# Kernel tuning notes

Hardware: AMD Instinct MI355X
Metric: run time of the kernel (lower is better)

## Reference

```python
import jax, jax.numpy as jnp
import numpy as np

# Module hyperparameters (match init_kwargs)
E, H = 16, 8          # embedding_dim, n_head
DI, DO = 8, 8         # dim_in, dim_out (voices)
F = 48                # num_frames_in = num_frames_out = max_num_frames
L_IN, L_OUT = F * DI, F * DO
SZ_B = 4              # batch size (q has SZ_B * H leading dim)


def _expand(mat):
    # mat: (F, F, E, H) -> (L_IN, L_OUT, E, H), block expansion over voices
    e = jnp.tile(mat, (1, DI, 1, 1))                 # (F, DI*F, E, H)
    f = e.reshape(DI * F, F, E, H)                   # (L_IN, F, E, H)
    g = jnp.transpose(f, (1, 0, 2, 3))               # (F, L_IN, E, H)
    h = jnp.tile(g, (1, DO, 1, 1))                   # (F, DO*L_IN, E, H)
    ret = jnp.transpose(h.reshape(DO * F, DI * F, E, H), (1, 0, 2, 3))
    return ret[:L_IN, :L_OUT]


def _prepare_r_time(inp, is_future):
    # inp: (F, E, H). Skewing trick via pad + tile + reshape (faithful to torch).
    a = jnp.concatenate([inp, jnp.full((1, E, H), -111.0, inp.dtype)], axis=0)  # (F+1, E, H)
    b = jnp.tile(a[None], (F, 1, 1, 1))              # (F, F+1, E, H)
    c = b.reshape(F + 1, F, E, H)
    d = c[:F] if is_future else jnp.transpose(c[:F], (1, 0, 2, 3))  # (F, F, E, H)
    return _expand(d)


def _preprocess(r_voice, e_past, e_future):
    one = jnp.ones((F, F), r_voice.dtype)
    mask_past = jnp.broadcast_to(jnp.tril(one)[:, :, None, None], (F, F, E, H))
    mask_future = jnp.broadcast_to(jnp.triu(one, 1)[:, :, None, None], (F, F, E, H))
    r_voice_rep = jnp.tile(r_voice, (F, F, 1, 1))    # (L_IN, L_OUT, E, H)
    r_time = (_expand(mask_past) * _prepare_r_time(e_past, False)
              + _expand(mask_future) * _prepare_r_time(e_future, True))
    return r_voice_rep, r_time


def setup_inputs() -> dict:
    key = jax.random.key(0)
    k1, k2, k3, k4 = jax.random.split(key, 4)
    return {
        "q": jax.random.normal(k1, (SZ_B * H, L_IN, E), jnp.float32),
        "flipped_masks": jnp.zeros((1,), jnp.int32),  # unused by forward
        "r_voice": jax.random.normal(k2, (DI, DO, E, H), jnp.float32),
        "e_past": jax.random.normal(k3, (F, E, H), jnp.float32),
        "e_future": jax.random.normal(k4, (F, E, H), jnp.float32),
    }


def reference(q, flipped_masks, r_voice, e_past, e_future):
    rv, rt = _preprocess(r_voice, e_past, e_future)
    # torch: permute(3,0,1,2) then repeat over batch -> (b*H, L, M, E) with index b*H + h.
    # Equivalent without the batch repeat: reshape q to (b, H, L, E) and einsum over heads.
    rv = jnp.transpose(rv, (3, 0, 1, 2))             # (H, L_IN, L_OUT, E)
    rt = jnp.transpose(rt, (3, 0, 1, 2))
    qb = q.reshape(SZ_B, H, L_IN, E)
    # use_voice_attention=True: rel_attn_instrument + rel_attn_time (single fused einsum)
    rel = jnp.einsum('bhld,hlmd->bhlm', qb, rv + rt)
    return rel.reshape(SZ_B * H, L_IN, L_OUT)
```

## Files before the change

kernel.cpp:

```cpp
#include <hip/hip_runtime.h>
#include <hip/hip_bf16.h>

#define E_DIM 16
#define H_DIM 8
#define F_DIM 48
#define L_IN 384
#define L_OUT 384
#define SZ_B 4

#define NCHUNK 8
#define ROWS_PER_BLOCK 48
#define FI_PER 6
#define TSTRIDE 20

typedef float f32x4 __attribute__((ext_vector_type(4)));

__global__ __launch_bounds__(512)
void bsa_fused_kernel(const float* __restrict__ q,
                      const float* __restrict__ r_voice,
                      const float* __restrict__ e_past,
                      const float* __restrict__ e_future,
                      float* __restrict__ out) {
    const int chunk = blockIdx.x;
    const int bh    = blockIdx.y;
    const int h     = bh & (H_DIM - 1);
    const int t     = threadIdx.x;
    const int w     = t >> 6;
    const int lane  = t & 63;

    __shared__ __attribute__((aligned(16))) float tabs[160 * TSTRIDE];
    __shared__ __attribute__((aligned(16))) float qs[ROWS_PER_BLOCK * E_DIM];
    __shared__ __attribute__((aligned(16))) float scratch[8 * 64];

    for (int i = t; i < F_DIM * E_DIM; i += 512) {
        const int f = i >> 4, d = i & 15;
        tabs[f * TSTRIDE + d]           = e_past [(size_t)i * H_DIM + h];
        tabs[(F_DIM + f) * TSTRIDE + d] = e_future[(size_t)i * H_DIM + h];
    }
    for (int i = t; i < 64 * E_DIM; i += 512) {
        const int r = i >> 4, d = i & 15;
        tabs[(96 + r) * TSTRIDE + d] = r_voice[(size_t)i * H_DIM + h];
    }
    for (int i = t; i < ROWS_PER_BLOCK * E_DIM; i += 512)
        qs[i] = q[((size_t)bh * L_IN + chunk * ROWS_PER_BLOCK) * E_DIM + i];
    __syncthreads();

    float* wscratch = &scratch[w * 64];

    for (int j = 0; j < FI_PER; ++j) {
        const int lrow = w * FI_PER + j;
        const int l    = chunk * ROWS_PER_BLOCK + lrow;
        const int fi   = l >> 3;
        const int vi   = l & 7;

        int r;
        if (lane < 48) {
            r = (lane <= fi) ? (fi - lane) : (F_DIM + lane - fi);
        } else {
            int vj = (lane - 48) & 7;
            r = 96 + vi * 8 + vj;
        }
        const f32x4* qv = (const f32x4*)&qs[lrow * E_DIM];
        const f32x4* tv = (const f32x4*)&tabs[r * TSTRIDE];
        f32x4 acc = qv[0] * tv[0] + qv[1] * tv[1] + qv[2] * tv[2] + qv[3] * tv[3];
        const float s = acc.x + acc.y + acc.z + acc.w;
        if (lane < 56) wscratch[lane] = s;
        asm volatile("s_waitcnt lgkmcnt(0)" ::: "memory");
        __builtin_amdgcn_wave_barrier();

        float* orow = out + ((size_t)bh * L_IN + l) * L_OUT;
        #pragma unroll
        for (int rr = 0; rr < 2; ++rr) {
            const int jj = rr * 64 + lane;
            if (jj < 96) {
                const float tval = wscratch[jj >> 1];
                const f32x4 vv = *(const f32x4*)&wscratch[48 + 4 * (jj & 1)];
                f32x4 o;
                o.x = tval + vv.x; o.y = tval + vv.y;
                o.z = tval + vv.z; o.w = tval + vv.w;
                __builtin_nontemporal_store(o, (f32x4*)(orow + 4 * jj));
            }
        }
        __builtin_amdgcn_wave_barrier();
    }
}

extern "C" void kernel_launch(void* const* d_in, const int* in_sizes, int n_in,
                              void* d_out, int out_size, void* d_ws, size_t ws_size,
                              hipStream_t stream) {
    const float* q        = (const float*)d_in[0];
    const float* r_voice  = (const float*)d_in[2];
    const float* e_past   = (const float*)d_in[3];
    const float* e_future = (const float*)d_in[4];
    float* out = (float*)d_out;

    dim3 grid(NCHUNK, SZ_B * H_DIM);
    bsa_fused_kernel<<<grid, dim3(512), 0, stream>>>(q, r_voice, e_past, e_future, out);
}
```

Before: 10.78 us.

## Halve block size, double grid, batch dot products before stores, drop nontemporal

Moves to 256-thread blocks covering 24 rows each, doubling the grid to 512 blocks so more CUs share the work. Each wave now computes all six rows' dot products into per-row scratch first, then does one wave barrier and issues all output stores, instead of alternating compute, barrier and store per row. Nontemporal stores are replaced by normal stores. In exchange, the per-head tables are loaded into LDS twice as many times overall, and losing the nontemporal hint may change how the output write stream interacts with the cache.

```diff
diff --git a/kernel.cpp b/kernel.cpp
--- a/kernel.cpp
+++ b/kernel.cpp
@@ -8,14 +8,14 @@
 #define L_OUT 384
 #define SZ_B 4
 
-#define NCHUNK 8
-#define ROWS_PER_BLOCK 48
-#define FI_PER 6
+#define NCHUNK 16
+#define ROWS_PER_BLOCK 24
+#define ROWS_PER_WAVE 6
 #define TSTRIDE 20
 
 typedef float f32x4 __attribute__((ext_vector_type(4)));
 
-__global__ __launch_bounds__(512)
+__global__ __launch_bounds__(256)
 void bsa_fused_kernel(const float* __restrict__ q,
                       const float* __restrict__ r_voice,
                       const float* __restrict__ e_past,
@@ -30,58 +30,62 @@
 
     __shared__ __attribute__((aligned(16))) float tabs[160 * TSTRIDE];
     __shared__ __attribute__((aligned(16))) float qs[ROWS_PER_BLOCK * E_DIM];
-    __shared__ __attribute__((aligned(16))) float scratch[8 * 64];
+    __shared__ __attribute__((aligned(16))) float scratch[4][ROWS_PER_WAVE * 64];
 
-    for (int i = t; i < F_DIM * E_DIM; i += 512) {
+    for (int i = t; i < F_DIM * E_DIM; i += 256) {
         const int f = i >> 4, d = i & 15;
         tabs[f * TSTRIDE + d]           = e_past [(size_t)i * H_DIM + h];
         tabs[(F_DIM + f) * TSTRIDE + d] = e_future[(size_t)i * H_DIM + h];
     }
-    for (int i = t; i < 64 * E_DIM; i += 512) {
+    for (int i = t; i < 64 * E_DIM; i += 256) {
         const int r = i >> 4, d = i & 15;
         tabs[(96 + r) * TSTRIDE + d] = r_voice[(size_t)i * H_DIM + h];
     }
-    for (int i = t; i < ROWS_PER_BLOCK * E_DIM; i += 512)
+    for (int i = t; i < ROWS_PER_BLOCK * E_DIM; i += 256)
         qs[i] = q[((size_t)bh * L_IN + chunk * ROWS_PER_BLOCK) * E_DIM + i];
     __syncthreads();
 
-    float* wscratch = &scratch[w * 64];
+    float* wscratch = scratch[w];
+    const int lbase = chunk * ROWS_PER_BLOCK + w * ROWS_PER_WAVE;
 
-    for (int j = 0; j < FI_PER; ++j) {
-        const int lrow = w * FI_PER + j;
-        const int l    = chunk * ROWS_PER_BLOCK + lrow;
+    #pragma unroll
+    for (int j = 0; j < ROWS_PER_WAVE; ++j) {
+        const int lrow = w * ROWS_PER_WAVE + j;
+        const int l    = lbase + j;
         const int fi   = l >> 3;
         const int vi   = l & 7;
-
         int r;
         if (lane < 48) {
             r = (lane <= fi) ? (fi - lane) : (F_DIM + lane - fi);
         } else {
-            int vj = (lane - 48) & 7;
-            r = 96 + vi * 8 + vj;
+            r = 96 + vi * 8 + ((lane - 48) & 7);
         }
         const f32x4* qv = (const f32x4*)&qs[lrow * E_DIM];
         const f32x4* tv = (const f32x4*)&tabs[r * TSTRIDE];
         f32x4 acc = qv[0] * tv[0] + qv[1] * tv[1] + qv[2] * tv[2] + qv[3] * tv[3];
         const float s = acc.x + acc.y + acc.z + acc.w;
-        if (lane < 56) wscratch[lane] = s;
-        asm volatile("s_waitcnt lgkmcnt(0)" ::: "memory");
-        __builtin_amdgcn_wave_barrier();
+        if (lane < 56) wscratch[j * 64 + lane] = s;
+    }
+    asm volatile("s_waitcnt lgkmcnt(0)" ::: "memory");
+    __builtin_amdgcn_wave_barrier();
 
+    #pragma unroll
+    for (int j = 0; j < ROWS_PER_WAVE; ++j) {
+        const int l = lbase + j;
         float* orow = out + ((size_t)bh * L_IN + l) * L_OUT;
+        const float* ws_ = &wscratch[j * 64];
         #pragma unroll
         for (int rr = 0; rr < 2; ++rr) {
             const int jj = rr * 64 + lane;
             if (jj < 96) {
-                const float tval = wscratch[jj >> 1];
-                const f32x4 vv = *(const f32x4*)&wscratch[48 + 4 * (jj & 1)];
+                const float tval = ws_[jj >> 1];
+                const f32x4 vv = *(const f32x4*)&ws_[48 + 4 * (jj & 1)];
                 f32x4 o;
                 o.x = tval + vv.x; o.y = tval + vv.y;
                 o.z = tval + vv.z; o.w = tval + vv.w;
-                __builtin_nontemporal_store(o, (f32x4*)(orow + 4 * jj));
+                *(f32x4*)(orow + 4 * jj) = o;
             }
         }
-        __builtin_amdgcn_wave_barrier();
     }
 }
 
@@ -95,5 +99,5 @@
     float* out = (float*)d_out;
 
     dim3 grid(NCHUNK, SZ_B * H_DIM);
-    bsa_fused_kernel<<<grid, dim3(512), 0, stream>>>(q, r_voice, e_past, e_future, out);
+    bsa_fused_kernel<<<grid, dim3(256), 0, stream>>>(q, r_voice, e_past, e_future, out);
 }
```

Result: slower. 13.28 us (+23.1%).
